# Performance work log

Measured on AMD Instinct MI355X. Metric: run time of the kernel, lower is better.

The kernel has to match this reference:

```python
import jax, jax.numpy as jnp
import numpy as np

B, S, D = 8, 1024, 768
H = 12
DH = D // H  # 64


def setup_inputs() -> dict:
    key = jax.random.key(0)
    ks = jax.random.split(key, 9)
    s = 0.02
    return {
        "x": jax.random.normal(ks[0], (B, S, D), dtype=jnp.float32),
        # per-head QKV projections stacked over heads: [H, D, DH]
        "Wq": jax.random.normal(ks[1], (H, D, DH), dtype=jnp.float32) * s,
        "bq": jax.random.normal(ks[2], (H, DH), dtype=jnp.float32) * s,
        "Wk": jax.random.normal(ks[3], (H, D, DH), dtype=jnp.float32) * s,
        "bk": jax.random.normal(ks[4], (H, DH), dtype=jnp.float32) * s,
        "Wv": jax.random.normal(ks[5], (H, D, DH), dtype=jnp.float32) * s,
        "bv": jax.random.normal(ks[6], (H, DH), dtype=jnp.float32) * s,
        # output projection: [D, D] (applied as x @ Wo + bo)
        "Wo": jax.random.normal(ks[7], (D, D), dtype=jnp.float32) * s,
        "bo": jax.random.normal(ks[8], (D,), dtype=jnp.float32) * s,
    }


def reference(x, Wq, bq, Wk, bk, Wv, bv, Wo, bo):
    # Per-head linear projections, vectorized over heads -> [B, H, S, DH]
    q = jnp.einsum("bsd,hde->bhse", x, Wq) + bq[None, :, None, :]
    k = jnp.einsum("bsd,hde->bhse", x, Wk) + bk[None, :, None, :]
    v = jnp.einsum("bsd,hde->bhse", x, Wv) + bv[None, :, None, :]
    scale = 1.0 / jnp.sqrt(jnp.asarray(DH, dtype=q.dtype))
    scores = jnp.einsum("bhse,bhte->bhst", q, k) * scale  # [B,H,S,S]
    probs = jax.nn.softmax(scores, axis=-1)  # dropout p=0 (eval)
    out = jnp.einsum("bhst,bhte->bhse", probs, v)  # [B,H,S,DH]
    # concat heads (head order matches ModuleList order) -> [B,S,D]
    out = out.transpose(0, 2, 1, 3).reshape(B, S, D)
    return out @ Wo + bo
```

## Files before the change

kernel.cpp:

```cpp
#include <hip/hip_runtime.h>
#include <math.h>

#define BB 8
#define SS 1024
#define DD 768
#define HH 12
#define DHH 64
#define BSS (BB*SS)
#define NQKV 2304

typedef _Float16 half8 __attribute__((ext_vector_type(8)));
typedef _Float16 half4 __attribute__((ext_vector_type(4)));
typedef float    f32x4 __attribute__((ext_vector_type(4)));

__device__ __forceinline__ void glds16(const _Float16* g, _Float16* l)
{
    __builtin_amdgcn_global_load_lds(
        (const __attribute__((address_space(1))) uint32_t*)(g),
        (__attribute__((address_space(3))) uint32_t*)(l),
        16, 0, 0);
}

__global__ __launch_bounds__(256)
void cast_x_f16(const float* __restrict__ x, _Float16* __restrict__ xh)
{
    int i = blockIdx.x * 256 + threadIdx.x;
    const float4* xp = (const float4*)x + (size_t)i * 2;
    float4 u = xp[0], v = xp[1];
    half8 h = { (_Float16)u.x, (_Float16)u.y, (_Float16)u.z, (_Float16)u.w,
                (_Float16)v.x, (_Float16)v.y, (_Float16)v.z, (_Float16)v.w };
    ((half8*)xh)[i] = h;
}

__device__ __forceinline__
void transpose_tile(const float* __restrict__ src, _Float16* __restrict__ dst,
                    int d0, int n_outer, int base_mul, int row_stride, int tid)
{
    __shared__ float T[64][65];
    const size_t base = (size_t)n_outer * base_mul;
    {
        int dl = tid >> 2, c0 = (tid & 3) * 16;
        const float* p = src + base + (size_t)(d0 + dl) * row_stride + c0;
#pragma unroll
        for (int m = 0; m < 4; ++m) {
            float4 f = *(const float4*)(p + m * 4);
            T[dl][c0 + m*4 + 0] = f.x;
            T[dl][c0 + m*4 + 1] = f.y;
            T[dl][c0 + m*4 + 2] = f.z;
            T[dl][c0 + m*4 + 3] = f.w;
        }
    }
    __syncthreads();
    {
        int e = tid >> 2, c = tid & 3;
        half8 lo, hi;
#pragma unroll
        for (int i = 0; i < 8; ++i) {
            lo[i] = (_Float16)T[c*16 + i][e];
            hi[i] = (_Float16)T[c*16 + 8 + i][e];
        }
        _Float16* q = dst + ((size_t)n_outer * 64 + e) * DD + d0 + c * 16;
        *(half8*)q = lo;
        *(half8*)(q + 8) = hi;
    }
}

__global__ __launch_bounds__(256)
void transpose_all(const float* __restrict__ Wq, const float* __restrict__ Wk,
                   const float* __restrict__ Wv, const float* __restrict__ Wo,
                   _Float16* __restrict__ Wt, _Float16* __restrict__ Wot)
{
    const int z = blockIdx.z;
    const float* src;
    _Float16* dst;
    int base_mul, row_stride;
    if (z < 3) {
        src = (z == 0) ? Wq : (z == 1) ? Wk : Wv;
        dst = Wt + (size_t)z * DD * DD;
        base_mul = DD * DHH; row_stride = DHH;
    } else {
        src = Wo; dst = Wot;
        base_mul = 64; row_stride = DD;
    }
    transpose_tile(src, dst, blockIdx.x * 64, blockIdx.y, base_mul, row_stride,
                   threadIdx.x);
}

__global__ __launch_bounds__(256)
void gemm_qkv_stacked(const _Float16* __restrict__ Xh, const _Float16* __restrict__ Wt,
                      const float* __restrict__ bq, const float* __restrict__ bk,
                      const float* __restrict__ bv,
                      _Float16* __restrict__ qo, _Float16* __restrict__ ko,
                      _Float16* __restrict__ vto)
{
    __shared__ _Float16 Ash[2][128][32];
    __shared__ _Float16 Bsh[2][128][32];

    const int b = blockIdx.x;
    const int c  = b & 7;
    const int g  = b >> 3;
    const int n_t = g % 18;
    const int m_t = (g / 18) * 8 + c;
    const int m0 = m_t * 128;
    const int n0 = n_t * 128;

    const int tid  = threadIdx.x;
    const int wave = tid >> 6;
    const int lane = tid & 63;
    const int l16  = tid & 15;
    const int quad = (tid >> 4) & 3;
    const int wy = wave >> 1;
    const int wx = wave & 1;

    const _Float16* ap = Xh + (size_t)(m0 + 32 * wave + (lane >> 2)) * DD + (lane & 3) * 8;
    const _Float16* bp = Wt + (size_t)(n0 + 32 * wave + (lane >> 2)) * DD + (lane & 3) * 8;

    f32x4 acc[4][4];
#pragma unroll
    for (int i = 0; i < 4; ++i)
#pragma unroll
        for (int j = 0; j < 4; ++j) acc[i][j] = (f32x4){0.f, 0.f, 0.f, 0.f};

    glds16(ap, &Ash[0][32 * wave][0]);
    glds16(ap + 16 * DD, &Ash[0][32 * wave + 16][0]);
    glds16(bp, &Bsh[0][32 * wave][0]);
    glds16(bp + 16 * DD, &Bsh[0][32 * wave + 16][0]);

    int cur = 0;
    for (int k0 = 0; k0 < DD; k0 += 32) {
        __syncthreads();
        if (k0 + 32 < DD) {
            glds16(ap + k0 + 32, &Ash[cur ^ 1][32 * wave][0]);
            glds16(ap + k0 + 32 + 16 * DD, &Ash[cur ^ 1][32 * wave + 16][0]);
            glds16(bp + k0 + 32, &Bsh[cur ^ 1][32 * wave][0]);
            glds16(bp + k0 + 32 + 16 * DD, &Bsh[cur ^ 1][32 * wave + 16][0]);
        }

        half8 a[4], bf[4];
#pragma unroll
        for (int i = 0; i < 4; ++i)
            a[i] = *(const half8*)&Ash[cur][wy * 64 + i * 16 + l16][quad * 8];
#pragma unroll
        for (int j = 0; j < 4; ++j)
            bf[j] = *(const half8*)&Bsh[cur][wx * 64 + j * 16 + l16][quad * 8];
#pragma unroll
        for (int i = 0; i < 4; ++i)
#pragma unroll
            for (int j = 0; j < 4; ++j)
                acc[i][j] = __builtin_amdgcn_mfma_f32_16x16x32_f16(a[i], bf[j], acc[i][j], 0, 0, 0);
        cur ^= 1;
    }

    const int w = n0 / 768;
    const float* bp_ = (w == 0) ? bq : (w == 1) ? bk : bv;
    const int nb = n0 - w * 768 + wx * 64;
    const float qscale = (w == 0) ? 0.125f : 1.0f;

#pragma unroll
    for (int i = 0; i < 4; ++i) {
#pragma unroll
        for (int r = 0; r < 4; ++r) {
            int row = m0 + wy * 64 + i * 16 + quad * 4 + r;
            int b_ = row >> 10;
            int s  = row & (SS - 1);
#pragma unroll
            for (int j = 0; j < 4; ++j) {
                int nl = nb + j * 16 + l16;
                int h = nl >> 6, e = nl & 63;
                float val = (acc[i][j][r] + bp_[nl]) * qscale;
                if (w == 0)
                    qo[((size_t)(b_ * HH + h) * SS + s) * DHH + e] = (_Float16)val;
                else if (w == 1)
                    ko[((size_t)(b_ * HH + h) * SS + s) * DHH + e] = (_Float16)val;
                else
                    vto[((size_t)(b_ * HH + h) * DHH + e) * SS + s] = (_Float16)val;
            }
        }
    }
}

__global__ __launch_bounds__(256)
void gemm_out_f16(const _Float16* __restrict__ Ah, const _Float16* __restrict__ Bt,
                  const float* __restrict__ bias, float* __restrict__ out)
{
    __shared__ _Float16 Ash[2][128][32];
    __shared__ _Float16 Bsh[2][64][32];

    const int m0 = blockIdx.x * 128;
    const int n0 = blockIdx.y * 64;
    const int tid  = threadIdx.x;
    const int wave = tid >> 6;
    const int lane = tid & 63;
    const int l16  = tid & 15;
    const int quad = (tid >> 4) & 3;
    const int wy = wave >> 1;
    const int wx = wave & 1;

    const _Float16* ap = Ah + (size_t)(m0 + 32 * wave + (lane >> 2)) * DD + (lane & 3) * 8;
    const _Float16* bp = Bt + (size_t)(n0 + 16 * wave + (lane >> 2)) * DD + (lane & 3) * 8;

    f32x4 acc[4][2];
#pragma unroll
    for (int i = 0; i < 4; ++i)
#pragma unroll
        for (int j = 0; j < 2; ++j) acc[i][j] = (f32x4){0.f, 0.f, 0.f, 0.f};

    glds16(ap, &Ash[0][32 * wave][0]);
    glds16(ap + 16 * DD, &Ash[0][32 * wave + 16][0]);
    glds16(bp, &Bsh[0][16 * wave][0]);

    int cur = 0;
    for (int k0 = 0; k0 < DD; k0 += 32) {
        __syncthreads();
        if (k0 + 32 < DD) {
            glds16(ap + k0 + 32, &Ash[cur ^ 1][32 * wave][0]);
            glds16(ap + k0 + 32 + 16 * DD, &Ash[cur ^ 1][32 * wave + 16][0]);
            glds16(bp + k0 + 32, &Bsh[cur ^ 1][16 * wave][0]);
        }

        half8 a[4], bf[2];
#pragma unroll
        for (int i = 0; i < 4; ++i)
            a[i] = *(const half8*)&Ash[cur][wy * 64 + i * 16 + l16][quad * 8];
#pragma unroll
        for (int j = 0; j < 2; ++j)
            bf[j] = *(const half8*)&Bsh[cur][wx * 32 + j * 16 + l16][quad * 8];
#pragma unroll
        for (int i = 0; i < 4; ++i)
#pragma unroll
            for (int j = 0; j < 2; ++j)
                acc[i][j] = __builtin_amdgcn_mfma_f32_16x16x32_f16(a[i], bf[j], acc[i][j], 0, 0, 0);
        cur ^= 1;
    }

#pragma unroll
    for (int i = 0; i < 4; ++i) {
#pragma unroll
        for (int r = 0; r < 4; ++r) {
            int row = m0 + wy * 64 + i * 16 + quad * 4 + r;
#pragma unroll
            for (int j = 0; j < 2; ++j) {
                int col = n0 + wx * 32 + j * 16 + l16;
                out[(size_t)row * DD + col] = acc[i][j][r] + bias[col];
            }
        }
    }
}

__global__ __launch_bounds__(512)
void attn_f16(const _Float16* __restrict__ qh, const _Float16* __restrict__ kh,
              const _Float16* __restrict__ vt, _Float16* __restrict__ ctxh)
{
    const int bh  = blockIdx.x;
    const int q0  = blockIdx.y * 128;
    const int tid = threadIdx.x;
    const int wave = tid >> 6;
    const int lane = tid & 63;
    const int l16  = tid & 15;
    const int quad = (tid >> 4) & 3;

    __shared__ _Float16 Ks[2][64][64];
    __shared__ _Float16 Vt[2][64][64];
    __shared__ _Float16 Pt[8][16][72];

    const _Float16* qrow = qh + ((size_t)bh * SS + q0 + wave * 16 + l16) * DHH;
    const half8 qlo = *(const half8*)(qrow + quad * 8);
    const half8 qhi = *(const half8*)(qrow + 32 + quad * 8);

    const _Float16* kp = kh + ((size_t)bh * SS + 8 * wave + (lane >> 3)) * DHH + (lane & 7) * 8;
    const _Float16* vp = vt + ((size_t)bh * DHH + 8 * wave + (lane >> 3)) * SS + (lane & 7) * 8;

    f32x4 o[4];
    float lacc = 0.f;
#pragma unroll
    for (int j = 0; j < 4; ++j) o[j] = (f32x4){0.f, 0.f, 0.f, 0.f};

    glds16(kp, &Ks[0][8 * wave][0]);
    glds16(vp, &Vt[0][8 * wave][0]);

    int cur = 0;
    for (int kt = 0; kt < SS; kt += 64) {
        __syncthreads();
        if (kt + 64 < SS) {
            glds16(kp + (size_t)(kt + 64) * DHH, &Ks[cur ^ 1][8 * wave][0]);
            glds16(vp + kt + 64, &Vt[cur ^ 1][8 * wave][0]);
        }

#pragma unroll
        for (int f = 0; f < 4; ++f) {
            half8 klo = *(const half8*)&Ks[cur][f * 16 + l16][quad * 8];
            half8 khi = *(const half8*)&Ks[cur][f * 16 + l16][32 + quad * 8];
            f32x4 z = (f32x4){0.f, 0.f, 0.f, 0.f};
            z = __builtin_amdgcn_mfma_f32_16x16x32_f16(klo, qlo, z, 0, 0, 0);
            z = __builtin_amdgcn_mfma_f32_16x16x32_f16(khi, qhi, z, 0, 0, 0);
            half4 pk;
#pragma unroll
            for (int r = 0; r < 4; ++r) {
                float p = __expf(z[r]);
                lacc += p;
                pk[r] = (_Float16)p;
            }
            *(half4*)&Pt[wave][l16][f * 16 + quad * 4] = pk;
        }

        half8 pl = *(const half8*)&Pt[wave][l16][quad * 8];
        half8 ph = *(const half8*)&Pt[wave][l16][32 + quad * 8];

#pragma unroll
        for (int j = 0; j < 4; ++j) {
            half8 vlo = *(const half8*)&Vt[cur][j * 16 + l16][quad * 8];
            half8 vhi = *(const half8*)&Vt[cur][j * 16 + l16][32 + quad * 8];
            o[j] = __builtin_amdgcn_mfma_f32_16x16x32_f16(pl, vlo, o[j], 0, 0, 0);
            o[j] = __builtin_amdgcn_mfma_f32_16x16x32_f16(ph, vhi, o[j], 0, 0, 0);
        }
        cur ^= 1;
    }

    float lr = lacc;
    lr += __shfl_xor(lr, 16);
    lr += __shfl_xor(lr, 32);

    const int b_ = bh / HH;
    const int h_ = bh % HH;
#pragma unroll
    for (int r = 0; r < 4; ++r) {
        float invl = 1.f / __shfl(lr, quad * 4 + r, 16);
        int s_ = q0 + wave * 16 + quad * 4 + r;
        _Float16* orow = ctxh + ((size_t)(b_ * SS + s_)) * DD + h_ * DHH;
#pragma unroll
        for (int j = 0; j < 4; ++j)
            orow[j * 16 + l16] = (_Float16)(o[j][r] * invl);
    }
}

extern "C" void kernel_launch(void* const* d_in, const int* in_sizes, int n_in,
                              void* d_out, int out_size, void* d_ws, size_t ws_size,
                              hipStream_t stream)
{
    const float* x  = (const float*)d_in[0];
    const float* Wq = (const float*)d_in[1];
    const float* bq = (const float*)d_in[2];
    const float* Wk = (const float*)d_in[3];
    const float* bk = (const float*)d_in[4];
    const float* Wv = (const float*)d_in[5];
    const float* bv = (const float*)d_in[6];
    const float* Wo = (const float*)d_in[7];
    const float* bo = (const float*)d_in[8];
    float* out = (float*)d_out;

    const size_t xe = (size_t)BSS * DD;
    const size_t we = (size_t)DD * DD;
    _Float16* Xh   = (_Float16*)d_ws;
    _Float16* Wt   = Xh  + xe;
    _Float16* Wot  = Wt  + (size_t)3 * we;
    _Float16* qhb  = Wot + we;
    _Float16* khb  = qhb + xe;
    _Float16* vtb  = khb + xe;
    _Float16* ctxh = vtb + xe;

    cast_x_f16<<<xe / 8 / 256, 256, 0, stream>>>(x, Xh);

    dim3 tg(DD / 64, DD / 64, 4);
    transpose_all<<<tg, 256, 0, stream>>>(Wq, Wk, Wv, Wo, Wt, Wot);

    gemm_qkv_stacked<<<(BSS / 128) * (NQKV / 128), 256, 0, stream>>>(
        Xh, Wt, bq, bk, bv, qhb, khb, vtb);

    dim3 ag(BB * HH, SS / 128);
    attn_f16<<<ag, 512, 0, stream>>>(qhb, khb, vtb, ctxh);

    dim3 gg(BSS / 128, DD / 64);
    gemm_out_f16<<<gg, 256, 0, stream>>>(ctxh, Wot, bo, out);
}
```

Measured before the change: 237.0 us.

## Merge prep kernels and widen QKV GEMM tile to 128x256

Folds the x cast and the weight transposes into a single prep launch, with block index ranges choosing the role, which removes one kernel launch. The QKV projection GEMM tile widens from 128x128 to 128x256. Each wave now accumulates a 64x128 block, which doubles the MFMA work per LDS load of A and halves the grid size. The costs are more accumulator registers (hence launch_bounds(256,2)), more shared memory for B, and fewer blocks to spread across the CUs.

```diff
diff --git a/kernel.cpp b/kernel.cpp
--- a/kernel.cpp
+++ b/kernel.cpp
@@ -22,55 +22,31 @@
 }
 
 __global__ __launch_bounds__(256)
-void cast_x_f16(const float* __restrict__ x, _Float16* __restrict__ xh)
-{
-    int i = blockIdx.x * 256 + threadIdx.x;
-    const float4* xp = (const float4*)x + (size_t)i * 2;
-    float4 u = xp[0], v = xp[1];
-    half8 h = { (_Float16)u.x, (_Float16)u.y, (_Float16)u.z, (_Float16)u.w,
-                (_Float16)v.x, (_Float16)v.y, (_Float16)v.z, (_Float16)v.w };
-    ((half8*)xh)[i] = h;
-}
-
-__device__ __forceinline__
-void transpose_tile(const float* __restrict__ src, _Float16* __restrict__ dst,
-                    int d0, int n_outer, int base_mul, int row_stride, int tid)
-{
+void prep(const float* __restrict__ x, _Float16* __restrict__ xh,
+          const float* __restrict__ Wq, const float* __restrict__ Wk,
+          const float* __restrict__ Wv, const float* __restrict__ Wo,
+          _Float16* __restrict__ Wt, _Float16* __restrict__ Wot)
+{
+    const int blk = blockIdx.x;
+    const int tid = threadIdx.x;
+
+    if (blk < 3072) {
+        int i = blk * 256 + tid;
+        const float4* xp = (const float4*)x + (size_t)i * 2;
+        float4 u = xp[0], v = xp[1];
+        half8 h = { (_Float16)u.x, (_Float16)u.y, (_Float16)u.z, (_Float16)u.w,
+                    (_Float16)v.x, (_Float16)v.y, (_Float16)v.z, (_Float16)v.w };
+        ((half8*)xh)[i] = h;
+        return;
+    }
+
     __shared__ float T[64][65];
-    const size_t base = (size_t)n_outer * base_mul;
-    {
-        int dl = tid >> 2, c0 = (tid & 3) * 16;
-        const float* p = src + base + (size_t)(d0 + dl) * row_stride + c0;
-#pragma unroll
-        for (int m = 0; m < 4; ++m) {
-            float4 f = *(const float4*)(p + m * 4);
-            T[dl][c0 + m*4 + 0] = f.x;
-            T[dl][c0 + m*4 + 1] = f.y;
-            T[dl][c0 + m*4 + 2] = f.z;
-            T[dl][c0 + m*4 + 3] = f.w;
-        }
-    }
-    __syncthreads();
-    {
-        int e = tid >> 2, c = tid & 3;
-        half8 lo, hi;
-#pragma unroll
-        for (int i = 0; i < 8; ++i) {
-            lo[i] = (_Float16)T[c*16 + i][e];
-            hi[i] = (_Float16)T[c*16 + 8 + i][e];
-        }
-        _Float16* q = dst + ((size_t)n_outer * 64 + e) * DD + d0 + c * 16;
-        *(half8*)q = lo;
-        *(half8*)(q + 8) = hi;
-    }
-}
-
-__global__ __launch_bounds__(256)
-void transpose_all(const float* __restrict__ Wq, const float* __restrict__ Wk,
-                   const float* __restrict__ Wv, const float* __restrict__ Wo,
-                   _Float16* __restrict__ Wt, _Float16* __restrict__ Wot)
-{
-    const int z = blockIdx.z;
+    const int t  = blk - 3072;
+    const int z  = t / 144;
+    const int r_ = t - z * 144;
+    const int d0 = (r_ / 12) * 64;
+    const int n_outer = r_ % 12;
+
     const float* src;
     _Float16* dst;
     int base_mul, row_stride;
@@ -82,11 +58,36 @@
         src = Wo; dst = Wot;
         base_mul = 64; row_stride = DD;
     }
-    transpose_tile(src, dst, blockIdx.x * 64, blockIdx.y, base_mul, row_stride,
-                   threadIdx.x);
-}
-
-__global__ __launch_bounds__(256)
+
+    const size_t base = (size_t)n_outer * base_mul;
+    {
+        int dl = tid >> 2, c0 = (tid & 3) * 16;
+        const float* p = src + base + (size_t)(d0 + dl) * row_stride + c0;
+#pragma unroll
+        for (int m = 0; m < 4; ++m) {
+            float4 f = *(const float4*)(p + m * 4);
+            T[dl][c0 + m*4 + 0] = f.x;
+            T[dl][c0 + m*4 + 1] = f.y;
+            T[dl][c0 + m*4 + 2] = f.z;
+            T[dl][c0 + m*4 + 3] = f.w;
+        }
+    }
+    __syncthreads();
+    {
+        int e = tid >> 2, c = tid & 3;
+        half8 lo, hi;
+#pragma unroll
+        for (int i = 0; i < 8; ++i) {
+            lo[i] = (_Float16)T[c*16 + i][e];
+            hi[i] = (_Float16)T[c*16 + 8 + i][e];
+        }
+        _Float16* q = dst + ((size_t)n_outer * 64 + e) * DD + d0 + c * 16;
+        *(half8*)q = lo;
+        *(half8*)(q + 8) = hi;
+    }
+}
+
+__global__ __launch_bounds__(256, 2)
 void gemm_qkv_stacked(const _Float16* __restrict__ Xh, const _Float16* __restrict__ Wt,
                       const float* __restrict__ bq, const float* __restrict__ bk,
                       const float* __restrict__ bv,
@@ -94,15 +95,15 @@
                       _Float16* __restrict__ vto)
 {
     __shared__ _Float16 Ash[2][128][32];
-    __shared__ _Float16 Bsh[2][128][32];
+    __shared__ _Float16 Bsh[2][256][32];
 
     const int b = blockIdx.x;
     const int c  = b & 7;
     const int g  = b >> 3;
-    const int n_t = g % 18;
-    const int m_t = (g / 18) * 8 + c;
+    const int n_t = g % 9;
+    const int m_t = (g / 9) * 8 + c;
     const int m0 = m_t * 128;
-    const int n0 = n_t * 128;
+    const int n0 = n_t * 256;
 
     const int tid  = threadIdx.x;
     const int wave = tid >> 6;
@@ -113,18 +114,19 @@
     const int wx = wave & 1;
 
     const _Float16* ap = Xh + (size_t)(m0 + 32 * wave + (lane >> 2)) * DD + (lane & 3) * 8;
-    const _Float16* bp = Wt + (size_t)(n0 + 32 * wave + (lane >> 2)) * DD + (lane & 3) * 8;
-
-    f32x4 acc[4][4];
+    const _Float16* bp = Wt + (size_t)(n0 + 64 * wave + (lane >> 2)) * DD + (lane & 3) * 8;
+
+    f32x4 acc[4][8];
 #pragma unroll
     for (int i = 0; i < 4; ++i)
 #pragma unroll
-        for (int j = 0; j < 4; ++j) acc[i][j] = (f32x4){0.f, 0.f, 0.f, 0.f};
+        for (int j = 0; j < 8; ++j) acc[i][j] = (f32x4){0.f, 0.f, 0.f, 0.f};
 
     glds16(ap, &Ash[0][32 * wave][0]);
     glds16(ap + 16 * DD, &Ash[0][32 * wave + 16][0]);
-    glds16(bp, &Bsh[0][32 * wave][0]);
-    glds16(bp + 16 * DD, &Bsh[0][32 * wave + 16][0]);
+#pragma unroll
+    for (int t = 0; t < 4; ++t)
+        glds16(bp + (size_t)(16 * t) * DD, &Bsh[0][64 * wave + 16 * t][0]);
 
     int cur = 0;
     for (int k0 = 0; k0 < DD; k0 += 32) {
@@ -132,28 +134,30 @@
         if (k0 + 32 < DD) {
             glds16(ap + k0 + 32, &Ash[cur ^ 1][32 * wave][0]);
             glds16(ap + k0 + 32 + 16 * DD, &Ash[cur ^ 1][32 * wave + 16][0]);
-            glds16(bp + k0 + 32, &Bsh[cur ^ 1][32 * wave][0]);
-            glds16(bp + k0 + 32 + 16 * DD, &Bsh[cur ^ 1][32 * wave + 16][0]);
-        }
-
-        half8 a[4], bf[4];
+#pragma unroll
+            for (int t = 0; t < 4; ++t)
+                glds16(bp + k0 + 32 + (size_t)(16 * t) * DD,
+                       &Bsh[cur ^ 1][64 * wave + 16 * t][0]);
+        }
+
+        half8 a[4], bf[8];
 #pragma unroll
         for (int i = 0; i < 4; ++i)
             a[i] = *(const half8*)&Ash[cur][wy * 64 + i * 16 + l16][quad * 8];
 #pragma unroll
-        for (int j = 0; j < 4; ++j)
-            bf[j] = *(const half8*)&Bsh[cur][wx * 64 + j * 16 + l16][quad * 8];
+        for (int j = 0; j < 8; ++j)
+            bf[j] = *(const half8*)&Bsh[cur][wx * 128 + j * 16 + l16][quad * 8];
 #pragma unroll
         for (int i = 0; i < 4; ++i)
 #pragma unroll
-            for (int j = 0; j < 4; ++j)
+            for (int j = 0; j < 8; ++j)
                 acc[i][j] = __builtin_amdgcn_mfma_f32_16x16x32_f16(a[i], bf[j], acc[i][j], 0, 0, 0);
         cur ^= 1;
     }
 
     const int w = n0 / 768;
     const float* bp_ = (w == 0) ? bq : (w == 1) ? bk : bv;
-    const int nb = n0 - w * 768 + wx * 64;
+    const int nb = (n0 - w * 768) + wx * 128;
     const float qscale = (w == 0) ? 0.125f : 1.0f;
 
 #pragma unroll
@@ -164,7 +168,7 @@
             int b_ = row >> 10;
             int s  = row & (SS - 1);
 #pragma unroll
-            for (int j = 0; j < 4; ++j) {
+            for (int j = 0; j < 8; ++j) {
                 int nl = nb + j * 16 + l16;
                 int h = nl >> 6, e = nl & 63;
                 float val = (acc[i][j][r] + bp_[nl]) * qscale;
@@ -358,12 +362,9 @@
     _Float16* vtb  = khb + xe;
     _Float16* ctxh = vtb + xe;
 
-    cast_x_f16<<<xe / 8 / 256, 256, 0, stream>>>(x, Xh);
-
-    dim3 tg(DD / 64, DD / 64, 4);
-    transpose_all<<<tg, 256, 0, stream>>>(Wq, Wk, Wv, Wo, Wt, Wot);
-
-    gemm_qkv_stacked<<<(BSS / 128) * (NQKV / 128), 256, 0, stream>>>(
+    prep<<<3072 + 576, 256, 0, stream>>>(x, Xh, Wq, Wk, Wv, Wo, Wt, Wot);
+
+    gemm_qkv_stacked<<<(BSS / 128) * (NQKV / 256), 256, 0, stream>>>(
         Xh, Wt, bq, bk, bv, qhb, khb, vtb);
 
     dim3 ag(BB * HH, SS / 128);
```

Result: slower. 248.7 us (+4.9%).

## Merge cast and transpose kernels; split attention K/V LDS tiles into halves

Applied to the files above, without the earlier changes.

Merges the x-cast and weight-transpose kernels into one prep launch, with block index ranges picking the work, which removes one kernel launch. In attention, K and V tiles are stored as two 32-wide halves so each LDS row is 64 bytes. Four waves now load K and four load V, each issuing two 16-byte loads per tile. The narrower rows are meant to cut LDS bank conflicts on the half8 reads, at the cost of more branching in the loader.

```diff
diff --git a/kernel.cpp b/kernel.cpp
--- a/kernel.cpp
+++ b/kernel.cpp
@@ -22,55 +22,31 @@
 }
 
 __global__ __launch_bounds__(256)
-void cast_x_f16(const float* __restrict__ x, _Float16* __restrict__ xh)
-{
-    int i = blockIdx.x * 256 + threadIdx.x;
-    const float4* xp = (const float4*)x + (size_t)i * 2;
-    float4 u = xp[0], v = xp[1];
-    half8 h = { (_Float16)u.x, (_Float16)u.y, (_Float16)u.z, (_Float16)u.w,
-                (_Float16)v.x, (_Float16)v.y, (_Float16)v.z, (_Float16)v.w };
-    ((half8*)xh)[i] = h;
-}
-
-__device__ __forceinline__
-void transpose_tile(const float* __restrict__ src, _Float16* __restrict__ dst,
-                    int d0, int n_outer, int base_mul, int row_stride, int tid)
-{
+void prep(const float* __restrict__ x, _Float16* __restrict__ xh,
+          const float* __restrict__ Wq, const float* __restrict__ Wk,
+          const float* __restrict__ Wv, const float* __restrict__ Wo,
+          _Float16* __restrict__ Wt, _Float16* __restrict__ Wot)
+{
+    const int blk = blockIdx.x;
+    const int tid = threadIdx.x;
+
+    if (blk < 3072) {
+        int i = blk * 256 + tid;
+        const float4* xp = (const float4*)x + (size_t)i * 2;
+        float4 u = xp[0], v = xp[1];
+        half8 h = { (_Float16)u.x, (_Float16)u.y, (_Float16)u.z, (_Float16)u.w,
+                    (_Float16)v.x, (_Float16)v.y, (_Float16)v.z, (_Float16)v.w };
+        ((half8*)xh)[i] = h;
+        return;
+    }
+
     __shared__ float T[64][65];
-    const size_t base = (size_t)n_outer * base_mul;
-    {
-        int dl = tid >> 2, c0 = (tid & 3) * 16;
-        const float* p = src + base + (size_t)(d0 + dl) * row_stride + c0;
-#pragma unroll
-        for (int m = 0; m < 4; ++m) {
-            float4 f = *(const float4*)(p + m * 4);
-            T[dl][c0 + m*4 + 0] = f.x;
-            T[dl][c0 + m*4 + 1] = f.y;
-            T[dl][c0 + m*4 + 2] = f.z;
-            T[dl][c0 + m*4 + 3] = f.w;
-        }
-    }
-    __syncthreads();
-    {
-        int e = tid >> 2, c = tid & 3;
-        half8 lo, hi;
-#pragma unroll
-        for (int i = 0; i < 8; ++i) {
-            lo[i] = (_Float16)T[c*16 + i][e];
-            hi[i] = (_Float16)T[c*16 + 8 + i][e];
-        }
-        _Float16* q = dst + ((size_t)n_outer * 64 + e) * DD + d0 + c * 16;
-        *(half8*)q = lo;
-        *(half8*)(q + 8) = hi;
-    }
-}
-
-__global__ __launch_bounds__(256)
-void transpose_all(const float* __restrict__ Wq, const float* __restrict__ Wk,
-                   const float* __restrict__ Wv, const float* __restrict__ Wo,
-                   _Float16* __restrict__ Wt, _Float16* __restrict__ Wot)
-{
-    const int z = blockIdx.z;
+    const int t  = blk - 3072;
+    const int z  = t / 144;
+    const int r_ = t - z * 144;
+    const int d0 = (r_ / 12) * 64;
+    const int n_outer = r_ % 12;
+
     const float* src;
     _Float16* dst;
     int base_mul, row_stride;
@@ -82,8 +58,33 @@
         src = Wo; dst = Wot;
         base_mul = 64; row_stride = DD;
     }
-    transpose_tile(src, dst, blockIdx.x * 64, blockIdx.y, base_mul, row_stride,
-                   threadIdx.x);
+
+    const size_t base = (size_t)n_outer * base_mul;
+    {
+        int dl = tid >> 2, c0 = (tid & 3) * 16;
+        const float* p = src + base + (size_t)(d0 + dl) * row_stride + c0;
+#pragma unroll
+        for (int m = 0; m < 4; ++m) {
+            float4 f = *(const float4*)(p + m * 4);
+            T[dl][c0 + m*4 + 0] = f.x;
+            T[dl][c0 + m*4 + 1] = f.y;
+            T[dl][c0 + m*4 + 2] = f.z;
+            T[dl][c0 + m*4 + 3] = f.w;
+        }
+    }
+    __syncthreads();
+    {
+        int e = tid >> 2, c = tid & 3;
+        half8 lo, hi;
+#pragma unroll
+        for (int i = 0; i < 8; ++i) {
+            lo[i] = (_Float16)T[c*16 + i][e];
+            hi[i] = (_Float16)T[c*16 + 8 + i][e];
+        }
+        _Float16* q = dst + ((size_t)n_outer * 64 + e) * DD + d0 + c * 16;
+        *(half8*)q = lo;
+        *(half8*)(q + 8) = hi;
+    }
 }
 
 __global__ __launch_bounds__(256)
@@ -259,37 +260,48 @@
     const int l16  = tid & 15;
     const int quad = (tid >> 4) & 3;
 
-    __shared__ _Float16 Ks[2][64][64];
-    __shared__ _Float16 Vt[2][64][64];
+    __shared__ _Float16 Ks[2][2][64][32];
+    __shared__ _Float16 Vt[2][2][64][32];
     __shared__ _Float16 Pt[8][16][72];
 
     const _Float16* qrow = qh + ((size_t)bh * SS + q0 + wave * 16 + l16) * DHH;
     const half8 qlo = *(const half8*)(qrow + quad * 8);
     const half8 qhi = *(const half8*)(qrow + 32 + quad * 8);
 
-    const _Float16* kp = kh + ((size_t)bh * SS + 8 * wave + (lane >> 3)) * DHH + (lane & 7) * 8;
-    const _Float16* vp = vt + ((size_t)bh * DHH + 8 * wave + (lane >> 3)) * SS + (lane & 7) * 8;
+    const int sw = wave & 3;
+    const _Float16* kp = kh + ((size_t)bh * SS + 16 * sw + (lane >> 2)) * DHH + (lane & 3) * 8;
+    const _Float16* vp = vt + ((size_t)bh * DHH + 16 * sw + (lane >> 2)) * SS + (lane & 3) * 8;
 
     f32x4 o[4];
     float lacc = 0.f;
 #pragma unroll
     for (int j = 0; j < 4; ++j) o[j] = (f32x4){0.f, 0.f, 0.f, 0.f};
 
-    glds16(kp, &Ks[0][8 * wave][0]);
-    glds16(vp, &Vt[0][8 * wave][0]);
+    if (wave < 4) {
+        glds16(kp,      &Ks[0][0][16 * sw][0]);
+        glds16(kp + 32, &Ks[0][1][16 * sw][0]);
+    } else {
+        glds16(vp,      &Vt[0][0][16 * sw][0]);
+        glds16(vp + 32, &Vt[0][1][16 * sw][0]);
+    }
 
     int cur = 0;
     for (int kt = 0; kt < SS; kt += 64) {
         __syncthreads();
         if (kt + 64 < SS) {
-            glds16(kp + (size_t)(kt + 64) * DHH, &Ks[cur ^ 1][8 * wave][0]);
-            glds16(vp + kt + 64, &Vt[cur ^ 1][8 * wave][0]);
+            if (wave < 4) {
+                glds16(kp + (size_t)(kt + 64) * DHH,      &Ks[cur ^ 1][0][16 * sw][0]);
+                glds16(kp + (size_t)(kt + 64) * DHH + 32, &Ks[cur ^ 1][1][16 * sw][0]);
+            } else {
+                glds16(vp + kt + 64,      &Vt[cur ^ 1][0][16 * sw][0]);
+                glds16(vp + kt + 64 + 32, &Vt[cur ^ 1][1][16 * sw][0]);
+            }
         }
 
 #pragma unroll
         for (int f = 0; f < 4; ++f) {
-            half8 klo = *(const half8*)&Ks[cur][f * 16 + l16][quad * 8];
-            half8 khi = *(const half8*)&Ks[cur][f * 16 + l16][32 + quad * 8];
+            half8 klo = *(const half8*)&Ks[cur][0][f * 16 + l16][quad * 8];
+            half8 khi = *(const half8*)&Ks[cur][1][f * 16 + l16][quad * 8];
             f32x4 z = (f32x4){0.f, 0.f, 0.f, 0.f};
             z = __builtin_amdgcn_mfma_f32_16x16x32_f16(klo, qlo, z, 0, 0, 0);
             z = __builtin_amdgcn_mfma_f32_16x16x32_f16(khi, qhi, z, 0, 0, 0);
@@ -308,8 +320,8 @@
 
 #pragma unroll
         for (int j = 0; j < 4; ++j) {
-            half8 vlo = *(const half8*)&Vt[cur][j * 16 + l16][quad * 8];
-            half8 vhi = *(const half8*)&Vt[cur][j * 16 + l16][32 + quad * 8];
+            half8 vlo = *(const half8*)&Vt[cur][0][j * 16 + l16][quad * 8];
+            half8 vhi = *(const half8*)&Vt[cur][1][j * 16 + l16][quad * 8];
             o[j] = __builtin_amdgcn_mfma_f32_16x16x32_f16(pl, vlo, o[j], 0, 0, 0);
             o[j] = __builtin_amdgcn_mfma_f32_16x16x32_f16(ph, vhi, o[j], 0, 0, 0);
         }
@@ -358,10 +370,7 @@
     _Float16* vtb  = khb + xe;
     _Float16* ctxh = vtb + xe;
 
-    cast_x_f16<<<xe / 8 / 256, 256, 0, stream>>>(x, Xh);
-
-    dim3 tg(DD / 64, DD / 64, 4);
-    transpose_all<<<tg, 256, 0, stream>>>(Wq, Wk, Wv, Wo, Wt, Wot);
+    prep<<<3072 + 576, 256, 0, stream>>>(x, Xh, Wq, Wk, Wv, Wo, Wt, Wot);
 
     gemm_qkv_stacked<<<(BSS / 128) * (NQKV / 128), 256, 0, stream>>>(
         Xh, Wt, bq, bk, bv, qhb, khb, vtb);
```

After: 213.7 us. 9.8% less time.
